# Performance work log

Measured on AMD Instinct MI355X. Metric: run time of the kernel, lower is better.

## Reference

```python
import jax, jax.numpy as jnp
import numpy as np

G_RATIO = 0.5
TMAX = 0.25
TB_FACTOR = 0.001


def conv2d(x, w, b):
    # x: [B,C,H,W], w: [O,C,kh,kw]
    y = jax.lax.conv_general_dilated(x, w, (1, 1), 'SAME',
                                     dimension_numbers=('NCHW', 'OIHW', 'NCHW'))
    return y + b[None, :, None, None]


def encoder(inputs, w1, b1, w2, b2):
    # simplified cost-map encoder standing in for smp.Unet; outputs sigmoid cost map [B,1,H,W]
    h = jax.nn.relu(conv2d(inputs, w1, b1))
    return jax.nn.sigmoid(conv2d(h, w2, b2))


def get_heuristic(goal_maps, tb_factor=TB_FACTOR):
    # goal_maps: [B,H,W] one-hot
    B, H, W = goal_maps.shape
    yy, xx = jnp.meshgrid(jnp.arange(H), jnp.arange(W), indexing='ij')
    loc = jnp.stack([yy, xx], 0).astype(goal_maps.dtype)          # [2,H,W]
    goal_loc = jnp.einsum('kij,bij->bk', loc, goal_maps)           # [B,2]
    d = jnp.abs(loc[None] - goal_loc[:, :, None, None])            # [B,2,H,W]
    h = d.min(axis=1) + d.max(axis=1)                              # chebyshev-style
    euc = jnp.sqrt((d ** 2).sum(axis=1))
    return h + tb_factor * euc


def st_softmax_noexp(val):
    # straight-through hard selection of the max-probability node
    B = val.shape[0]
    v = val.reshape(B, -1)
    y = v / v.sum(-1, keepdims=True)
    ind = jnp.argmax(y, axis=-1)
    y_hard = jax.nn.one_hot(ind, y.shape[-1], dtype=y.dtype)
    return (jax.lax.stop_gradient(y_hard - y) + y).reshape(val.shape)


def backtrack(start_maps, goal_maps, parents, current_t):
    B, H, W = start_maps.shape
    par = jax.lax.stop_gradient(parents).astype(jnp.int32)         # [B,HW]
    goal_flat = goal_maps.reshape(B, -1).astype(jnp.int32)
    path = goal_flat
    loc = (par * goal_flat).sum(-1)                                # parent of goal node
    rng = jnp.arange(B)

    def body(i, carry):
        path, loc = carry
        path = path.at[rng, loc].set(1)
        loc = par[rng, loc]
        return (path, loc)

    path, _ = jax.lax.fori_loop(0, current_t, body, (path, loc))
    return path.reshape(B, H, W).astype(jnp.float32)


def differentiable_astar(cost_maps, start_maps, goal_maps, obstacles_maps):
    cost = cost_maps[:, 0]
    start = start_maps[:, 0]
    goal = goal_maps[:, 0]
    obs = obstacles_maps[:, 0]
    B, H, W = cost.shape

    # Moore (8-neighbor) expansion filter: 3x3 ones with zero center
    nf = jnp.ones((1, 1, 3, 3), cost.dtype).at[0, 0, 1, 1].set(0.0)

    def expand(x):  # x: [B,H,W]
        return jax.lax.conv_general_dilated(x[:, None], nf, (1, 1), 'SAME',
                                            dimension_numbers=('NCHW', 'OIHW', 'NCHW'))[:, 0]

    h = get_heuristic(goal) + cost
    size = W
    steps = int(TMAX * H * W)
    inv_sqrt = 1.0 / np.sqrt(size)

    goal_idx = jnp.argmax(goal.reshape(B, -1), -1).astype(cost.dtype)
    parents0 = jnp.broadcast_to(goal_idx[:, None], (B, H * W)).astype(cost.dtype)
    one = jnp.asarray(1.0, cost.dtype)

    def step(carry, _):
        g, open_m, hist, parents = carry
        f = G_RATIO * g + (1.0 - G_RATIO) * h
        f_exp = jnp.exp(-f * inv_sqrt) * open_m
        sel = st_softmax_noexp(f_exp)                              # [B,H,W]

        dist_to_goal = (sel * goal).sum((1, 2), keepdims=True)
        is_unsolved = (dist_to_goal < 1e-8).astype(cost.dtype)

        hist = jnp.clip(hist + sel, 0.0, 1.0)
        open_m = jnp.clip(open_m - is_unsolved * sel, 0.0, 1.0)

        nbr = expand(sel) * obs
        g2 = expand((g + cost) * sel)
        idx = ((one - open_m) * (one - hist) + open_m * (g > g2).astype(cost.dtype)) * nbr
        idx = jax.lax.stop_gradient(idx)
        g = g2 * idx + g * (one - idx)
        g = jax.lax.stop_gradient(g)                               # detach_g=True
        open_m = jax.lax.stop_gradient(jnp.clip(open_m + idx, 0.0, 1.0))

        idx_f = idx.reshape(B, -1)
        new_par = jnp.argmax(sel.reshape(B, -1), -1).astype(cost.dtype)[:, None]
        parents = new_par * idx_f + parents * (one - idx_f)
        return (g, open_m, hist, parents), None

    init = (jnp.zeros_like(cost), start, jnp.zeros_like(cost), parents0)
    (g, open_m, hist, parents), _ = jax.lax.scan(step, init, None, length=steps)

    paths = backtrack(start, goal, parents, steps - 1)
    return hist[:, None], paths[:, None]


def setup_inputs() -> dict:
    key = jax.random.key(0)
    k1, k2, k3, k4, k5 = jax.random.split(key, 5)
    B, H, W = 64, 32, 32
    maps = (jax.random.uniform(k1, (B, 1, H, W)) > 0.15).astype(jnp.float32)  # 1 = free
    sidx = jax.random.randint(k2, (B,), 0, H * W)
    gidx = jax.random.randint(k3, (B,), 0, H * W)
    start = jax.nn.one_hot(sidx, H * W, dtype=jnp.float32).reshape(B, 1, H, W)
    goal = jax.nn.one_hot(gidx, H * W, dtype=jnp.float32).reshape(B, 1, H, W)
    maps = jnp.clip(maps + start + goal, 0.0, 1.0)  # ensure start/goal are free
    w1 = jax.random.normal(k4, (32, 2, 3, 3), jnp.float32) * 0.1
    b1 = jnp.zeros((32,), jnp.float32)
    w2 = jax.random.normal(k5, (1, 32, 3, 3), jnp.float32) * 0.1
    b2 = jnp.zeros((1,), jnp.float32)
    return {"map_designs": maps, "start_maps": start, "goal_maps": goal,
            "w1": w1, "b1": b1, "w2": w2, "b2": b2}


def reference(map_designs, start_maps, goal_maps, w1, b1, w2, b2):
    # encoder_input='m+': concat map with start+goal
    inputs = jnp.concatenate([map_designs, start_maps + goal_maps], axis=1)
    pred_cost_maps = encoder(inputs, w1, b1, w2, b2)
    obstacles_maps = map_designs  # ignore_obstacles=True, learn_obstacles=False
    histories, paths = differentiable_astar(pred_cost_maps, start_maps, goal_maps, obstacles_maps)
    return histories, paths, pred_cost_maps
```

## Files before the change

kernel.cpp:

```cpp
#include <hip/hip_runtime.h>


#define HW 1024

#define DPP_MAX64(key, ctrl) do {                                              \
    unsigned int _lo = (unsigned int)(key);                                    \
    unsigned int _hi = (unsigned int)((key) >> 32);                            \
    unsigned int _slo = (unsigned int)__builtin_amdgcn_update_dpp(             \
        (int)_lo, (int)_lo, (ctrl), 0xf, 0xf, false);                          \
    unsigned int _shi = (unsigned int)__builtin_amdgcn_update_dpp(             \
        (int)_hi, (int)_hi, (ctrl), 0xf, 0xf, false);                          \
    unsigned long long _o = ((unsigned long long)_shi << 32) | _slo;           \
    if (_o > (key)) (key) = _o;                                                \
} while (0)

__global__ __launch_bounds__(256) void fused_nastar(
    const float* __restrict__ maps, const float* __restrict__ start,
    const float* __restrict__ goal, const float* __restrict__ w1,
    const float* __restrict__ b1, const float* __restrict__ w2,
    const float* __restrict__ b2, float* __restrict__ out_hist,
    float* __restrict__ out_path, float* __restrict__ out_cost) {
  __shared__ float hid[8][HW];
  __shared__ float c_l[HW];
  __shared__ unsigned short par[HW];
  __shared__ unsigned char path_sh[HW];
  __shared__ unsigned int hist_lds[64];

  const int t = threadIdx.x;
  const int b = blockIdx.x;
  const float C_INV = 0.17677669529663687f;

  const float* m_p = maps  + b * HW;
  const float* s_p = start + b * HW;
  const float* g_p = goal  + b * HW;

  float acc2[4] = {b2[0], b2[0], b2[0], b2[0]};
  for (int grp = 0; grp < 4; ++grp) {
    #pragma unroll
    for (int p = 0; p < 4; ++p) {
      int pix = p * 256 + t;
      int y = pix >> 5, x = pix & 31;
      float win0[9], win1[9];
      #pragma unroll
      for (int ky = 0; ky < 3; ++ky) {
        #pragma unroll
        for (int kx = 0; kx < 3; ++kx) {
          int yy = y + ky - 1, xx = x + kx - 1;
          bool ok = (yy >= 0) && (yy <= 31) && (xx >= 0) && (xx <= 31);
          int q = ok ? yy * 32 + xx : 0;
          float v0 = m_p[q];
          float v1 = s_p[q] + g_p[q];
          win0[ky * 3 + kx] = ok ? v0 : 0.0f;
          win1[ky * 3 + kx] = ok ? v1 : 0.0f;
        }
      }
      #pragma unroll
      for (int ocl = 0; ocl < 8; ++ocl) {
        int oc = grp * 8 + ocl;
        const float* w = w1 + oc * 18;
        float acc = b1[oc];
        #pragma unroll
        for (int k = 0; k < 9; ++k) {
          acc += win0[k] * w[k];
          acc += win1[k] * w[9 + k];
        }
        hid[ocl][pix] = fmaxf(acc, 0.0f);
      }
    }
    __syncthreads();
    #pragma unroll
    for (int p = 0; p < 4; ++p) {
      int pix = p * 256 + t;
      int y = pix >> 5, x = pix & 31;
      float a = acc2[p];
      #pragma unroll
      for (int ocl = 0; ocl < 8; ++ocl) {
        int ic = grp * 8 + ocl;
        const float* w = w2 + ic * 9;
        #pragma unroll
        for (int ky = 0; ky < 3; ++ky) {
          #pragma unroll
          for (int kx = 0; kx < 3; ++kx) {
            int yy = y + ky - 1, xx = x + kx - 1;
            bool ok = (yy >= 0) && (yy <= 31) && (xx >= 0) && (xx <= 31);
            int q = ok ? yy * 32 + xx : 0;
            float hv = hid[ocl][q];
            a += (ok ? hv : 0.0f) * w[ky * 3 + kx];
          }
        }
      }
      acc2[p] = a;
    }
    __syncthreads();
  }
  #pragma unroll
  for (int p = 0; p < 4; ++p) {
    int pix = p * 256 + t;
    float c = 1.0f / (1.0f + expf(-acc2[p]));
    c_l[pix] = c;
    out_cost[b * HW + pix] = c;
  }
  __syncthreads();

  if (t < 64) {
    const int lane = t;
    reinterpret_cast<int4*>(path_sh)[lane] = make_int4(0, 0, 0, 0);
    int myg = -1;
    #pragma unroll
    for (int j = 0; j < 16; ++j) {
      int cell = j * 64 + lane;
      if (g_p[cell] > 0.5f) myg = cell;
    }
    unsigned long long gm = __ballot(myg >= 0);
    int src_lane = (int)__ffsll(gm) - 1;
    const int goal_idx = __shfl(myg, src_lane, 64);
    const int gy = goal_idx >> 5, gx = goal_idx & 31;

    unsigned int open_m = 0, hist_m = 0, obs_m = 0;
    float gr[16], hr[16], cr[16];
    unsigned int vr[16];
    #pragma unroll
    for (int j = 0; j < 16; ++j) {
      int cell = j * 64 + lane;
      int y = cell >> 5, x = cell & 31;
      float cst = c_l[cell];
      cr[j] = cst;
      int dy = y - gy; dy = dy < 0 ? -dy : dy;
      int dx = x - gx; dx = dx < 0 ? -dx : dx;
      float e = sqrtf((float)(dy * dy + dx * dx));
      float heur = __fadd_rn((float)(dy + dx), __fmul_rn(0.001f, e));
      float hc = __fadd_rn(heur, cst);
      hr[j] = hc;
      gr[j] = 0.0f;
      bool isobs = (m_p[cell] != 0.0f);
      bool isst  = (s_p[cell] > 0.5f);
      if (isobs) obs_m  |= 1u << j;
      if (isst)  open_m |= 1u << j;
      float f = 0.5f * (0.0f + hc);
      float ex = expf(__fmul_rn(-f, C_INV));
      vr[j] = isst ? __float_as_uint(ex) : 0u;
      par[cell] = (unsigned short)goal_idx;
    }

    const int x = lane & 31, half = lane >> 5;
    const unsigned int lowbase = 1023u - (unsigned)lane;

    for (int step = 0; step < 256; ++step) {
      unsigned int tv[8], tj[8];
      #pragma unroll
      for (int i = 0; i < 8; ++i) {
        bool gt2 = vr[i + 8] > vr[i];
        tv[i] = gt2 ? vr[i + 8] : vr[i];
        tj[i] = gt2 ? (unsigned)(i + 8) : (unsigned)i;
      }
      #pragma unroll
      for (int s = 4; s >= 1; s >>= 1) {
        #pragma unroll
        for (int i = 0; i < s; ++i)
          if (tv[i + s] > tv[i]) { tv[i] = tv[i + s]; tj[i] = tj[i + s]; }
      }
      unsigned long long key = ((unsigned long long)tv[0] << 32) |
                               (unsigned long long)(lowbase - (tj[0] << 6));
      DPP_MAX64(key, 0x111);
      DPP_MAX64(key, 0x112);
      DPP_MAX64(key, 0x114);
      DPP_MAX64(key, 0x118);
      DPP_MAX64(key, 0x142);
      DPP_MAX64(key, 0x143);
      unsigned int klo =
          (unsigned int)__builtin_amdgcn_readlane((int)(unsigned int)key, 63);
      const int sel = __builtin_amdgcn_readfirstlane(1023 - (int)klo);
      const int jsel = sel >> 6, owner = sel & 63;
      const int ys = sel >> 5, xs = sel & 31;
      const bool unsolved = (sel != goal_idx);

      const int j0  = (ys > 0 ? ys - 1 : 0) >> 1;
      const int j1u = (j0 < 15) ? j0 + 1 : 15;
      const int jP  = (ys < 31 ? ys + 1 : 31) >> 1;
      const bool jS_is_j0 = (jsel == j0);
      const bool jP_is_j0 = (jP == j0);

      float gj0 = 0.f, hj0 = 0.f, cj0 = 0.f, gj1 = 0.f, hj1 = 0.f, cj1 = 0.f;
      #pragma unroll
      for (int j = 0; j < 16; ++j) {
        if (j0 == j) {
          const int jn = (j < 15) ? j + 1 : 15;
          gj0 = gr[j];  hj0 = hr[j];  cj0 = cr[j];
          gj1 = gr[jn]; hj1 = hr[jn]; cj1 = cr[jn];
        }
      }

      float gselv = jS_is_j0 ? gj0 : gj1;
      float cselv = jS_is_j0 ? cj0 : cj1;
      float gs = __uint_as_float((unsigned int)__builtin_amdgcn_readlane(
          (int)__float_as_uint(gselv), owner));
      float cs = __uint_as_float((unsigned int)__builtin_amdgcn_readlane(
          (int)__float_as_uint(cselv), owner));
      const float gsum = gs + cs;

      int dxs = x - xs; int adx = dxs < 0 ? -dxs : dxs;
      const bool act = (adx <= 1);
      const bool samep = (((ys ^ half) & 1) == 0);
      const int yA = samep ? ys : (ys - 1);
      const bool vAv = act && (samep ? (adx >= 1) : (yA >= 0));
      const int yB = ys + 1;
      const bool vBv = act && (!samep) && (yB <= 31);
      const int cA = vAv ? (yA * 32 + x) : 0;
      const int cB = vBv ? (yB * 32 + x) : 0;

      const bool vjA_is_j0 = (!samep) || jS_is_j0;
      const int vjA = samep ? jsel : j0;
      float gA = vjA_is_j0 ? gj0 : gj1;
      float hA = vjA_is_j0 ? hj0 : hj1;
      float gB = jP_is_j0 ? gj0 : gj1;
      float hB = jP_is_j0 ? hj0 : hj1;

      bool obA = (obs_m  >> (vjA & 15)) & 1;
      bool opA = (open_m >> (vjA & 15)) & 1;
      bool hiA = (hist_m >> (vjA & 15)) & 1;
      bool obB = (obs_m  >> (jP & 15)) & 1;
      bool opB = (open_m >> (jP & 15)) & 1;
      bool hiB = (hist_m >> (jP & 15)) & 1;

      const bool idxA = vAv && obA && ((!opA && !hiA) || (opA && (gA > gsum)));
      const bool idxB = vBv && obB && ((!opB && !hiB) || (opB && (gB > gsum)));
      const bool ownerlane = (lane == owner);
      const bool closeU = unsolved && ownerlane;

      const bool histnew = ownerlane && !((hist_m >> (jsel & 15)) & 1);
      const bool opencl  = closeU && ((open_m >> (jsel & 15)) & 1);

      hist_m |= ownerlane ? (1u << (jsel & 15)) : 0u;
      unsigned int clr = closeU ? (1u << (jsel & 15)) : 0u;
      unsigned int aA  = idxA ? (1u << (vjA & 15)) : 0u;
      unsigned int aB  = idxB ? (1u << (jP & 15)) : 0u;
      open_m = (open_m & ~clr) | aA | aB;

      float fA = 0.5f * (gsum + hA);
      unsigned int nvA = __float_as_uint(expf(__fmul_rn(-fA, C_INV)));
      float fB = 0.5f * (gsum + hB);
      unsigned int nvB = __float_as_uint(expf(__fmul_rn(-fB, C_INV)));

      if (idxA) par[cA] = (unsigned short)sel;
      if (idxB) par[cB] = (unsigned short)sel;

      #pragma unroll
      for (int j = 0; j < 16; ++j) {
        const bool hit = (j == j0) || (j == j1u);
        if (hit) {
          const bool atlo = (j == j0);
          const bool uA = idxA && (vjA_is_j0 == atlo);
          const bool uB = idxB && (jP_is_j0 == atlo);
          const bool uu = uA || uB;
          if (uu) gr[j] = gsum;
          unsigned int nv = uA ? nvA : nvB;
          if (uu) vr[j] = nv;
          if (j == jsel) {
            if (closeU) vr[j] = 0u;
          }
        }
      }

      unsigned long long anych = __ballot(idxA || idxB || histnew || opencl);
      if (anych == 0ull) break;
    }

    hist_lds[lane] = hist_m;

    if (lane == 0) {
      path_sh[goal_idx] = 1;
      int loc = par[goal_idx];
      for (int i = 0; i < 255; ++i) {
        if (path_sh[loc]) break;
        path_sh[loc] = 1;
        loc = par[loc];
      }
    }
  }
  __syncthreads();

  const int base = t * 4;
  float hv[4], pv[4];
  #pragma unroll
  for (int p = 0; p < 4; ++p) {
    int cell = base + p;
    hv[p] = (float)((hist_lds[cell & 63] >> (cell >> 6)) & 1);
    pv[p] = (float)path_sh[cell];
  }
  *reinterpret_cast<float4*>(out_hist + b * HW + base) =
      make_float4(hv[0], hv[1], hv[2], hv[3]);
  *reinterpret_cast<float4*>(out_path + b * HW + base) =
      make_float4(pv[0], pv[1], pv[2], pv[3]);
}

extern "C" void kernel_launch(void* const* d_in, const int* in_sizes, int n_in,
                              void* d_out, int out_size, void* d_ws, size_t ws_size,
                              hipStream_t stream) {
  (void)in_sizes; (void)n_in; (void)d_ws; (void)ws_size; (void)out_size;
  const float* maps  = (const float*)d_in[0];
  const float* start = (const float*)d_in[1];
  const float* goal  = (const float*)d_in[2];
  const float* w1    = (const float*)d_in[3];
  const float* b1    = (const float*)d_in[4];
  const float* w2    = (const float*)d_in[5];
  const float* b2    = (const float*)d_in[6];

  float* out      = (float*)d_out;
  float* out_hist = out;
  float* out_path = out + 64 * HW;
  float* out_cost = out + 128 * HW;

  fused_nastar<<<64, 256, 0, stream>>>(maps, start, goal, w1, b1, w2, b2,
                                       out_hist, out_path, out_cost);
}
```

Measured before the change: 156.1 us.

## Maintain incremental per-lane tournament tree and split argmax into two 32-bit DPP reductions

Each lane keeps a persistent tournament tree (pairs, quads, octs, root) over its 16 open-node values. Only the affected leaves are repaired after each expansion, so the full 16-element max is no longer rebuilt every step. The 64-bit packed DPP max reduction is replaced by two 32-bit DPP reductions: one for the max value, then one for the lowest index among lanes holding that value. This lowers the per-step serial latency of the A* loop, but the tree adds register pressure and the update code now sits inside the unrolled j0-select branch.

```diff
diff --git a/kernel.cpp b/kernel.cpp
--- a/kernel.cpp
+++ b/kernel.cpp
@@ -3,16 +3,23 @@
 
 #define HW 1024
 
-#define DPP_MAX64(key, ctrl) do {                                              \
-    unsigned int _lo = (unsigned int)(key);                                    \
-    unsigned int _hi = (unsigned int)((key) >> 32);                            \
-    unsigned int _slo = (unsigned int)__builtin_amdgcn_update_dpp(             \
-        (int)_lo, (int)_lo, (ctrl), 0xf, 0xf, false);                          \
-    unsigned int _shi = (unsigned int)__builtin_amdgcn_update_dpp(             \
-        (int)_hi, (int)_hi, (ctrl), 0xf, 0xf, false);                          \
-    unsigned long long _o = ((unsigned long long)_shi << 32) | _slo;           \
-    if (_o > (key)) (key) = _o;                                                \
+#define DPPMAX32(v, ctrl) do {                                                 \
+    unsigned int _s = (unsigned int)__builtin_amdgcn_update_dpp(               \
+        (int)(v), (int)(v), (ctrl), 0xf, 0xf, false);                          \
+    (v) = (_s > (v)) ? _s : (v);                                               \
 } while (0)
+
+#define PAIR_FIX(a_) { bool _r = vr[2*(a_)+1] > vr[2*(a_)];                    \
+    pv[(a_)] = _r ? vr[2*(a_)+1] : vr[2*(a_)];                                 \
+    pj[(a_)] = _r ? (unsigned)(2*(a_)+1) : (unsigned)(2*(a_)); }
+#define QUAD_FIX(q_) { bool _r = pv[2*(q_)+1] > pv[2*(q_)];                    \
+    qv[(q_)] = _r ? pv[2*(q_)+1] : pv[2*(q_)];                                 \
+    qj[(q_)] = _r ? pj[2*(q_)+1] : pj[2*(q_)]; }
+#define OCT_FIX(o_) { bool _r = qv[2*(o_)+1] > qv[2*(o_)];                     \
+    ov[(o_)] = _r ? qv[2*(o_)+1] : qv[2*(o_)];                                 \
+    oj[(o_)] = _r ? qj[2*(o_)+1] : qj[2*(o_)]; }
+#define ROOT_FIX() { bool _r = ov[1] > ov[0];                                  \
+    rv = _r ? ov[1] : ov[0]; rj = _r ? oj[1] : oj[0]; }
 
 __global__ __launch_bounds__(256) void fused_nastar(
     const float* __restrict__ maps, const float* __restrict__ start,
@@ -142,61 +149,46 @@
       par[cell] = (unsigned short)goal_idx;
     }
 
+    unsigned int pv[8], pj[8], qv[4], qj[4], ov[2], oj[2], rv, rj;
+    #pragma unroll
+    for (int a = 0; a < 8; ++a) PAIR_FIX(a);
+    #pragma unroll
+    for (int q = 0; q < 4; ++q) QUAD_FIX(q);
+    #pragma unroll
+    for (int o = 0; o < 2; ++o) OCT_FIX(o);
+    ROOT_FIX();
+
     const int x = lane & 31, half = lane >> 5;
     const unsigned int lowbase = 1023u - (unsigned)lane;
 
     for (int step = 0; step < 256; ++step) {
-      unsigned int tv[8], tj[8];
-      #pragma unroll
-      for (int i = 0; i < 8; ++i) {
-        bool gt2 = vr[i + 8] > vr[i];
-        tv[i] = gt2 ? vr[i + 8] : vr[i];
-        tj[i] = gt2 ? (unsigned)(i + 8) : (unsigned)i;
-      }
-      #pragma unroll
-      for (int s = 4; s >= 1; s >>= 1) {
-        #pragma unroll
-        for (int i = 0; i < s; ++i)
-          if (tv[i + s] > tv[i]) { tv[i] = tv[i + s]; tj[i] = tj[i + s]; }
-      }
-      unsigned long long key = ((unsigned long long)tv[0] << 32) |
-                               (unsigned long long)(lowbase - (tj[0] << 6));
-      DPP_MAX64(key, 0x111);
-      DPP_MAX64(key, 0x112);
-      DPP_MAX64(key, 0x114);
-      DPP_MAX64(key, 0x118);
-      DPP_MAX64(key, 0x142);
-      DPP_MAX64(key, 0x143);
-      unsigned int klo =
-          (unsigned int)__builtin_amdgcn_readlane((int)(unsigned int)key, 63);
+      unsigned int vmx = rv;
+      DPPMAX32(vmx, 0x111);
+      DPPMAX32(vmx, 0x112);
+      DPPMAX32(vmx, 0x114);
+      DPPMAX32(vmx, 0x118);
+      DPPMAX32(vmx, 0x142);
+      DPPMAX32(vmx, 0x143);
+      const unsigned int svmax =
+          (unsigned int)__builtin_amdgcn_readlane((int)vmx, 63);
+      unsigned int lo = (rv == svmax) ? (lowbase - (rj << 6)) : 0u;
+      DPPMAX32(lo, 0x111);
+      DPPMAX32(lo, 0x112);
+      DPPMAX32(lo, 0x114);
+      DPPMAX32(lo, 0x118);
+      DPPMAX32(lo, 0x142);
+      DPPMAX32(lo, 0x143);
+      const unsigned int klo =
+          (unsigned int)__builtin_amdgcn_readlane((int)lo, 63);
       const int sel = __builtin_amdgcn_readfirstlane(1023 - (int)klo);
       const int jsel = sel >> 6, owner = sel & 63;
       const int ys = sel >> 5, xs = sel & 31;
       const bool unsolved = (sel != goal_idx);
 
-      const int j0  = (ys > 0 ? ys - 1 : 0) >> 1;
-      const int j1u = (j0 < 15) ? j0 + 1 : 15;
-      const int jP  = (ys < 31 ? ys + 1 : 31) >> 1;
+      const int j0 = (ys > 0 ? ys - 1 : 0) >> 1;
+      const int jP = (ys < 31 ? ys + 1 : 31) >> 1;
       const bool jS_is_j0 = (jsel == j0);
       const bool jP_is_j0 = (jP == j0);
-
-      float gj0 = 0.f, hj0 = 0.f, cj0 = 0.f, gj1 = 0.f, hj1 = 0.f, cj1 = 0.f;
-      #pragma unroll
-      for (int j = 0; j < 16; ++j) {
-        if (j0 == j) {
-          const int jn = (j < 15) ? j + 1 : 15;
-          gj0 = gr[j];  hj0 = hr[j];  cj0 = cr[j];
-          gj1 = gr[jn]; hj1 = hr[jn]; cj1 = cr[jn];
-        }
-      }
-
-      float gselv = jS_is_j0 ? gj0 : gj1;
-      float cselv = jS_is_j0 ? cj0 : cj1;
-      float gs = __uint_as_float((unsigned int)__builtin_amdgcn_readlane(
-          (int)__float_as_uint(gselv), owner));
-      float cs = __uint_as_float((unsigned int)__builtin_amdgcn_readlane(
-          (int)__float_as_uint(cselv), owner));
-      const float gsum = gs + cs;
 
       int dxs = x - xs; int adx = dxs < 0 ? -dxs : dxs;
       const bool act = (adx <= 1);
@@ -207,13 +199,8 @@
       const bool vBv = act && (!samep) && (yB <= 31);
       const int cA = vAv ? (yA * 32 + x) : 0;
       const int cB = vBv ? (yB * 32 + x) : 0;
-
+      const int vjA = samep ? jsel : j0;
       const bool vjA_is_j0 = (!samep) || jS_is_j0;
-      const int vjA = samep ? jsel : j0;
-      float gA = vjA_is_j0 ? gj0 : gj1;
-      float hA = vjA_is_j0 ? hj0 : hj1;
-      float gB = jP_is_j0 ? gj0 : gj1;
-      float hB = jP_is_j0 ? hj0 : hj1;
 
       bool obA = (obs_m  >> (vjA & 15)) & 1;
       bool opA = (open_m >> (vjA & 15)) & 1;
@@ -221,45 +208,73 @@
       bool obB = (obs_m  >> (jP & 15)) & 1;
       bool opB = (open_m >> (jP & 15)) & 1;
       bool hiB = (hist_m >> (jP & 15)) & 1;
-
-      const bool idxA = vAv && obA && ((!opA && !hiA) || (opA && (gA > gsum)));
-      const bool idxB = vBv && obB && ((!opB && !hiB) || (opB && (gB > gsum)));
+      const bool canAn = vAv && obA && !opA && !hiA;
+      const bool canAr = vAv && obA && opA;
+      const bool canBn = vBv && obB && !opB && !hiB;
+      const bool canBr = vBv && obB && opB;
+
       const bool ownerlane = (lane == owner);
       const bool closeU = unsolved && ownerlane;
-
       const bool histnew = ownerlane && !((hist_m >> (jsel & 15)) & 1);
       const bool opencl  = closeU && ((open_m >> (jsel & 15)) & 1);
+
+      bool idxA = false, idxB = false;
+
+      #pragma unroll
+      for (int j = 0; j < 16; ++j) {
+        if (j0 == j) {
+          const int jn = (j < 15) ? j + 1 : 15;
+          const float gj0 = gr[j],  hj0v = hr[j],  cj0 = cr[j];
+          const float gj1 = gr[jn], hj1v = hr[jn], cj1 = cr[jn];
+          float gselv = jS_is_j0 ? gj0 : gj1;
+          float cselv = jS_is_j0 ? cj0 : cj1;
+          float gs = __uint_as_float((unsigned int)__builtin_amdgcn_readlane(
+              (int)__float_as_uint(gselv), owner));
+          float cs = __uint_as_float((unsigned int)__builtin_amdgcn_readlane(
+              (int)__float_as_uint(cselv), owner));
+          const float gsum = gs + cs;
+
+          const float gA = vjA_is_j0 ? gj0 : gj1;
+          const float hA = vjA_is_j0 ? hj0v : hj1v;
+          const float gB = jP_is_j0 ? gj0 : gj1;
+          const float hB = jP_is_j0 ? hj0v : hj1v;
+          idxA = canAn || (canAr && (gA > gsum));
+          idxB = canBn || (canBr && (gB > gsum));
+
+          float fA = 0.5f * (gsum + hA);
+          unsigned int nvA = __float_as_uint(expf(__fmul_rn(-fA, C_INV)));
+          float fB = 0.5f * (gsum + hB);
+          unsigned int nvB = __float_as_uint(expf(__fmul_rn(-fB, C_INV)));
+
+          const bool uA0 = idxA && vjA_is_j0, uB0 = idxB && jP_is_j0;
+          const bool uA1 = idxA && !vjA_is_j0, uB1 = idxB && !jP_is_j0;
+          const bool u0 = uA0 || uB0, u1 = uA1 || uB1;
+          if (u0) { gr[j]  = gsum; vr[j]  = uA0 ? nvA : nvB; }
+          if (u1) { gr[jn] = gsum; vr[jn] = uA1 ? nvA : nvB; }
+          if (closeU &&  jS_is_j0) vr[j]  = 0u;
+          if (closeU && !jS_is_j0) vr[jn] = 0u;
+
+          const int pa = j >> 1, pb = jn >> 1;
+          PAIR_FIX(pa);
+          if (pb != pa) PAIR_FIX(pb);
+          const int qa = pa >> 1, qb = pb >> 1;
+          QUAD_FIX(qa);
+          if (qb != qa) QUAD_FIX(qb);
+          const int oa = qa >> 1, ob = qb >> 1;
+          OCT_FIX(oa);
+          if (ob != oa) OCT_FIX(ob);
+          ROOT_FIX();
+        }
+      }
+
+      if (idxA) par[cA] = (unsigned short)sel;
+      if (idxB) par[cB] = (unsigned short)sel;
 
       hist_m |= ownerlane ? (1u << (jsel & 15)) : 0u;
       unsigned int clr = closeU ? (1u << (jsel & 15)) : 0u;
       unsigned int aA  = idxA ? (1u << (vjA & 15)) : 0u;
       unsigned int aB  = idxB ? (1u << (jP & 15)) : 0u;
       open_m = (open_m & ~clr) | aA | aB;
-
-      float fA = 0.5f * (gsum + hA);
-      unsigned int nvA = __float_as_uint(expf(__fmul_rn(-fA, C_INV)));
-      float fB = 0.5f * (gsum + hB);
-      unsigned int nvB = __float_as_uint(expf(__fmul_rn(-fB, C_INV)));
-
-      if (idxA) par[cA] = (unsigned short)sel;
-      if (idxB) par[cB] = (unsigned short)sel;
-
-      #pragma unroll
-      for (int j = 0; j < 16; ++j) {
-        const bool hit = (j == j0) || (j == j1u);
-        if (hit) {
-          const bool atlo = (j == j0);
-          const bool uA = idxA && (vjA_is_j0 == atlo);
-          const bool uB = idxB && (jP_is_j0 == atlo);
-          const bool uu = uA || uB;
-          if (uu) gr[j] = gsum;
-          unsigned int nv = uA ? nvA : nvB;
-          if (uu) vr[j] = nv;
-          if (j == jsel) {
-            if (closeU) vr[j] = 0u;
-          }
-        }
-      }
 
       unsigned long long anych = __ballot(idxA || idxB || histnew || opencl);
       if (anych == 0ull) break;
@@ -280,17 +295,17 @@
   __syncthreads();
 
   const int base = t * 4;
-  float hv[4], pv[4];
+  float hv[4], pvv[4];
   #pragma unroll
   for (int p = 0; p < 4; ++p) {
     int cell = base + p;
     hv[p] = (float)((hist_lds[cell & 63] >> (cell >> 6)) & 1);
-    pv[p] = (float)path_sh[cell];
+    pvv[p] = (float)path_sh[cell];
   }
   *reinterpret_cast<float4*>(out_hist + b * HW + base) =
       make_float4(hv[0], hv[1], hv[2], hv[3]);
   *reinterpret_cast<float4*>(out_path + b * HW + base) =
-      make_float4(pv[0], pv[1], pv[2], pv[3]);
+      make_float4(pvv[0], pvv[1], pvv[2], pvv[3]);
 }
 
 extern "C" void kernel_launch(void* const* d_in, const int* in_sizes, int n_in,
```

Result: faster. 141.4 us (-9.4%).
